# Kernel optimization log

Measured on AMD Instinct MI355X. Metric: run time of the kernel, lower is better.

## Reference

```python
import jax, jax.numpy as jnp
import numpy as np
import math

L = 16
LOGT = 19
T = 2 ** LOGT
F = 2
NMIN = 16
NMAX = 2048
X_MIN = 0.0
X_MAX = 1.0
N_POINTS = 524288
P1 = np.uint32(2654435761)  # spatial hash prime for y
P2 = np.uint32(805459861)   # spatial hash prime for z


def setup_inputs() -> dict:
    key = jax.random.key(0)
    k1, k2 = jax.random.split(key)
    x = jax.random.uniform(k1, (N_POINTS, 3), dtype=jnp.float32)
    hashmap = jax.random.normal(k2, (L, T, F), dtype=jnp.float32) * 1e-2
    b = math.exp((math.log(NMAX) - math.log(NMIN)) / (L - 1))
    resolution = jnp.asarray(np.floor(NMIN * b ** np.arange(L)), dtype=jnp.float32)
    return {"x": x, "hashmap": hashmap, "resolution": resolution}


def reference(x, hashmap, resolution):
    # normalize coords to [0,1] (x_min=0, x_max=1 here)
    xn = (x - X_MIN) / (X_MAX - X_MIN)
    # per-level scaled coords: [L, n, 3]
    xs = xn[None, :, :] * resolution[:, None, None]
    x0f = jnp.floor(xs)
    w = xs - x0f                                 # trilinear weights [L, n, 3]
    c0 = x0f.astype(jnp.uint32)
    c1 = c0 + jnp.uint32(1)
    hx0, hy0, hz0 = c0[..., 0], c0[..., 1] * P1, c0[..., 2] * P2
    hx1, hy1, hz1 = c1[..., 0], c1[..., 1] * P1, c1[..., 2] * P2
    Tm = jnp.uint32(T - 1)
    # 8 corner hash indices, order 000,001,010,011,100,101,110,111: [L, n, 8]
    idx = jnp.stack([
        (hx0 ^ hy0 ^ hz0) & Tm, (hx0 ^ hy0 ^ hz1) & Tm,
        (hx0 ^ hy1 ^ hz0) & Tm, (hx0 ^ hy1 ^ hz1) & Tm,
        (hx1 ^ hy0 ^ hz0) & Tm, (hx1 ^ hy0 ^ hz1) & Tm,
        (hx1 ^ hy1 ^ hz0) & Tm, (hx1 ^ hy1 ^ hz1) & Tm,
    ], axis=-1).astype(jnp.int32)
    wx, wy, wz = w[..., 0], w[..., 1], w[..., 2]
    wxn, wyn, wzn = 1.0 - wx, 1.0 - wy, 1.0 - wz
    # corner weights matching idx order: [L, n, 8]
    cw = jnp.stack([
        wxn * wyn * wzn, wxn * wyn * wz, wxn * wy * wzn, wxn * wy * wz,
        wx * wyn * wzn, wx * wyn * wz, wx * wy * wzn, wx * wy * wz,
    ], axis=-1)
    # gather per-level corner features: [L, n, 8, F]
    feats = jax.vmap(lambda h, i: h[i])(hashmap, idx)
    # interpolate and lay out as [n, L*F] (level-major, matching kernel store)
    out = jnp.einsum('lnc,lncf->nlf', cw, feats)
    return out.reshape(x.shape[0], L * F)
```

## Files before the change

kernel.cpp:

```cpp
#include <hip/hip_runtime.h>
#include <hip/hip_fp16.h>

namespace {
constexpr unsigned kT  = 1u << 19;
constexpr unsigned kTm = kT - 1u;
constexpr unsigned kP1 = 2654435761u;
constexpr unsigned kP2 = 805459861u;
constexpr int      kNPTS = 524288;

constexpr int      kD[5]        = {17, 23, 31, 43, 59};
constexpr unsigned kCellBase[6] = {0u, 4913u, 17080u, 46871u, 126378u, 331757u};
constexpr unsigned kDenseElems4 = 126378u * 8u;
constexpr unsigned kDenseElems5 = 331757u * 8u;
constexpr size_t   kStageBytes  = (size_t)kNPTS * 16u * 8u;
constexpr size_t   kDenseOff    = kStageBytes;
constexpr size_t   kWsNeedB     = kDenseOff + (size_t)kDenseElems4 * 4u;
constexpr size_t   kWsNeedA     = kDenseOff + (size_t)kDenseElems5 * 4u;

constexpr int kDBLK[2]       = {2048, 2560};
constexpr unsigned kMaxBlkV[2] = {3447, 3283};
constexpr int kHSeg[2][8][3][3] = {
 {
  {{ 4,   0,1399},{-1,0,0},{-1,0,0}},
  {{ 4,1399,2048},{ 5,0,2048},{ 6,0, 614}},
  {{ 6, 614,2048},{ 7,0,1877},{-1,0,0}},
  {{ 7,1877,2048},{ 8,0,2048},{ 9,0,1092}},
  {{ 9,1092,2048},{10,0,2048},{11,0, 307}},
  {{11, 307,2048},{12,0,1570},{-1,0,0}},
  {{12,1570,2048},{13,0,2048},{14,0, 785}},
  {{14, 785,2048},{15,0,2048},{-1,0,0}},
 },
 {
  {{ 5,   0, 723},{-1,0,0},{-1,0,0}},
  {{ 5, 723,2048},{ 6,0,1790},{-1,0,0}},
  {{ 6,1790,2048},{ 7,0,2048},{ 8,0, 809}},
  {{ 8, 809,2048},{ 9,0,1876},{-1,0,0}},
  {{ 9,1876,2048},{10,0,2048},{11,0, 895}},
  {{11, 895,2048},{12,0,1962},{-1,0,0}},
  {{12,1962,2048},{13,0,2048},{14,0, 981}},
  {{14, 981,2048},{15,0,2048},{-1,0,0}},
 }};
}

typedef float    f32x2 __attribute__((ext_vector_type(2)));
typedef float    f32x4 __attribute__((ext_vector_type(4)));
typedef unsigned u32x4 __attribute__((ext_vector_type(4)));

__device__ inline f32x2 h2_to_f2(unsigned w) {
    __half2 h = __builtin_bit_cast(__half2, w);
    f32x2 r; r.x = __half2float(h.x); r.y = __half2float(h.y);
    return r;
}

__global__ __launch_bounds__(256) void build_dense16(
    const float* __restrict__ hashmap, unsigned* __restrict__ dense16,
    unsigned elems)
{
    unsigned t = blockIdx.x * 256 + threadIdx.x;
    if (t >= elems) return;
    unsigned cell = t >> 3, corner = t & 7u;
    int l; unsigned rem;
    if      (cell < kCellBase[1]) { l = 0; rem = cell; }
    else if (cell < kCellBase[2]) { l = 1; rem = cell - kCellBase[1]; }
    else if (cell < kCellBase[3]) { l = 2; rem = cell - kCellBase[2]; }
    else if (cell < kCellBase[4]) { l = 3; rem = cell - kCellBase[3]; }
    else                          { l = 4; rem = cell - kCellBase[4]; }
    unsigned D = (unsigned)kD[l];
    unsigned ck = rem % D, tmp = rem / D;
    unsigned cj = tmp % D,  ci = tmp / D;
    unsigned ii = ci + ((corner >> 2) & 1u);
    unsigned jj = cj + ((corner >> 1) & 1u);
    unsigned kk = ck + (corner & 1u);
    unsigned h = (ii ^ (jj * kP1) ^ (kk * kP2)) & kTm;
    f32x2 v = reinterpret_cast<const f32x2*>(hashmap)[(size_t)l * kT + h];
    __half2 p;
    p.x = __float2half_rn(v.x);
    p.y = __float2half_rn(v.y);
    dense16[t] = __builtin_bit_cast(unsigned, p);
}

template <int V>
__global__ __launch_bounds__(256) void hashgrid_gather(
    const float* __restrict__ x,
    const float* __restrict__ hashmap,
    const float* __restrict__ resolution,
    const unsigned* __restrict__ dense16,
    f32x2* __restrict__ stage)
{
    unsigned i = blockIdx.x;
    unsigned g = i & 7u;
    unsigned j = i >> 3;
    unsigned tid = threadIdx.x;

    if (g == 0u && j < (unsigned)kDBLK[V]) {
        unsigned dc0 = j * 4u;
        int l = (int)(dc0 >> 11);
        unsigned c0 = dc0 & 2047u;
        float res = resolution[l];
        unsigned D = (unsigned)kD[l];
        const unsigned* __restrict__ tbl = dense16 + (size_t)kCellBase[l] * 8u;

        #pragma unroll
        for (int p = 0; p < 4; ++p) {
            int n = (int)((c0 + (unsigned)p) * 256u + tid);
            float px = __builtin_nontemporal_load(&x[3*n+0]);
            float py = __builtin_nontemporal_load(&x[3*n+1]);
            float pz = __builtin_nontemporal_load(&x[3*n+2]);
            float xs = px*res, ys = py*res, zs = pz*res;
            float fx = floorf(xs), fy = floorf(ys), fz = floorf(zs);
            float wx = xs-fx, wy = ys-fy, wz = zs-fz;
            unsigned cx0 = (unsigned)fx, cy0 = (unsigned)fy, cz0 = (unsigned)fz;
            unsigned cell = (cx0 * D + cy0) * D + cz0;
            const u32x4* blk = reinterpret_cast<const u32x4*>(tbl + (size_t)cell * 8u);
            u32x4 lo = blk[0], hi = blk[1];
            f32x2 f000 = h2_to_f2(lo.x), f001 = h2_to_f2(lo.y);
            f32x2 f010 = h2_to_f2(lo.z), f011 = h2_to_f2(lo.w);
            f32x2 f100 = h2_to_f2(hi.x), f101 = h2_to_f2(hi.y);
            f32x2 f110 = h2_to_f2(hi.z), f111 = h2_to_f2(hi.w);

            float wxn = 1.f - wx, wyn = 1.f - wy, wzn = 1.f - wz;
            float w000 = wxn*wyn*wzn, w001 = wxn*wyn*wz;
            float w010 = wxn*wy *wzn, w011 = wxn*wy *wz;
            float w100 = wx *wyn*wzn, w101 = wx *wyn*wz;
            float w110 = wx *wy *wzn, w111 = wx *wy *wz;

            f32x2 o;
            o.x = w000*f000.x + w001*f001.x + w010*f010.x + w011*f011.x
                + w100*f100.x + w101*f101.x + w110*f110.x + w111*f111.x;
            o.y = w000*f000.y + w001*f001.y + w010*f010.y + w011*f011.y
                + w100*f100.y + w101*f101.y + w110*f110.y + w111*f111.y;
            __builtin_nontemporal_store(o, &stage[(size_t)l * kNPTS + n]);
        }
        return;
    }

    unsigned jj = (g == 0u) ? j - (unsigned)kDBLK[V] : j;
    int lvl = -1; unsigned chunk = 0, acc = 0;
    #pragma unroll
    for (int s = 0; s < 3; ++s) {
        int l0 = kHSeg[V][g][s][0];
        if (l0 < 0) break;
        unsigned beg = (unsigned)kHSeg[V][g][s][1];
        unsigned len = (unsigned)kHSeg[V][g][s][2] - beg;
        if (jj < acc + len) { lvl = l0; chunk = beg + (jj - acc); break; }
        acc += len;
    }
    if (lvl < 0) return;

    int n = (int)(chunk * 256u + tid);

    float px = __builtin_nontemporal_load(&x[3*n+0]);
    float py = __builtin_nontemporal_load(&x[3*n+1]);
    float pz = __builtin_nontemporal_load(&x[3*n+2]);
    float res = resolution[lvl];

    float xs = px*res, ys = py*res, zs = pz*res;
    float fx = floorf(xs), fy = floorf(ys), fz = floorf(zs);
    float wx = xs-fx, wy = ys-fy, wz = zs-fz;

    unsigned cx0 = (unsigned)fx, cy0 = (unsigned)fy, cz0 = (unsigned)fz;

    f32x2 f000, f001, f010, f011, f100, f101, f110, f111;

    unsigned hy0 = cy0 * kP1, hy1 = (cy0 + 1u) * kP1;
    unsigned hz0 = cz0 * kP2, hz1 = (cz0 + 1u) * kP2;
    unsigned hyz00 = hy0 ^ hz0, hyz01 = hy0 ^ hz1;
    unsigned hyz10 = hy1 ^ hz0, hyz11 = hy1 ^ hz1;
    const f32x2* __restrict__ tb =
        reinterpret_cast<const f32x2*>(hashmap) + (size_t)lvl * kT;

    if ((cx0 & 1u) == 0u) {
        const f32x4* __restrict__ tb4 = reinterpret_cast<const f32x4*>(tb);
        unsigned i00 = (cx0 ^ hyz00) & kTm;
        unsigned i01 = (cx0 ^ hyz01) & kTm;
        unsigned i10 = (cx0 ^ hyz10) & kTm;
        unsigned i11 = (cx0 ^ hyz11) & kTm;
        f32x4 q00 = tb4[i00 >> 1];
        f32x4 q01 = tb4[i01 >> 1];
        f32x4 q10 = tb4[i10 >> 1];
        f32x4 q11 = tb4[i11 >> 1];
        bool o0 = (i00 & 1u), o1 = (i01 & 1u), o2 = (i10 & 1u), o3 = (i11 & 1u);
        f000.x = o0 ? q00.z : q00.x; f000.y = o0 ? q00.w : q00.y;
        f100.x = o0 ? q00.x : q00.z; f100.y = o0 ? q00.y : q00.w;
        f001.x = o1 ? q01.z : q01.x; f001.y = o1 ? q01.w : q01.y;
        f101.x = o1 ? q01.x : q01.z; f101.y = o1 ? q01.y : q01.w;
        f010.x = o2 ? q10.z : q10.x; f010.y = o2 ? q10.w : q10.y;
        f110.x = o2 ? q10.x : q10.z; f110.y = o2 ? q10.y : q10.w;
        f011.x = o3 ? q11.z : q11.x; f011.y = o3 ? q11.w : q11.y;
        f111.x = o3 ? q11.x : q11.z; f111.y = o3 ? q11.y : q11.w;
    } else {
        unsigned hx0 = cx0, hx1 = cx0 + 1u;
        f000 = tb[(hx0 ^ hyz00) & kTm];
        f001 = tb[(hx0 ^ hyz01) & kTm];
        f010 = tb[(hx0 ^ hyz10) & kTm];
        f011 = tb[(hx0 ^ hyz11) & kTm];
        f100 = tb[(hx1 ^ hyz00) & kTm];
        f101 = tb[(hx1 ^ hyz01) & kTm];
        f110 = tb[(hx1 ^ hyz10) & kTm];
        f111 = tb[(hx1 ^ hyz11) & kTm];
    }

    float wxn = 1.f - wx, wyn = 1.f - wy, wzn = 1.f - wz;
    float w000 = wxn*wyn*wzn, w001 = wxn*wyn*wz;
    float w010 = wxn*wy *wzn, w011 = wxn*wy *wz;
    float w100 = wx *wyn*wzn, w101 = wx *wyn*wz;
    float w110 = wx *wy *wzn, w111 = wx *wy *wz;

    f32x2 o;
    o.x = w000*f000.x + w001*f001.x + w010*f010.x + w011*f011.x
        + w100*f100.x + w101*f101.x + w110*f110.x + w111*f111.x;
    o.y = w000*f000.y + w001*f001.y + w010*f010.y + w011*f011.y
        + w100*f100.y + w101*f101.y + w110*f110.y + w111*f111.y;

    __builtin_nontemporal_store(o, &stage[(size_t)lvl * kNPTS + n]);
}

__global__ __launch_bounds__(256) void stage_transpose(
    const f32x2* __restrict__ stage, f32x4* __restrict__ out4)
{
    __shared__ f32x2 tile[128][17];
    unsigned n0 = blockIdx.x * 128u;
    unsigned t = threadIdx.x;

    #pragma unroll
    for (int it = 0; it < 8; ++it) {
        unsigned m = (unsigned)it * 256u + t;
        unsigned l = m >> 7, p = m & 127u;
        tile[p][l] = stage[(size_t)l * kNPTS + n0 + p];
    }
    __syncthreads();

    #pragma unroll
    for (int it = 0; it < 4; ++it) {
        unsigned v = (unsigned)it * 256u + t;
        unsigned p = v >> 3, q = v & 7u;
        f32x2 a = tile[p][2u*q], b = tile[p][2u*q + 1u];
        f32x4 w; w.x = a.x; w.y = a.y; w.z = b.x; w.w = b.y;
        __builtin_nontemporal_store(w, &out4[(size_t)(n0 + p) * 8u + q]);
    }
}

__global__ __launch_bounds__(256) void hashgrid_fwd_lvl(
    const float* __restrict__ x,
    const float* __restrict__ hashmap,
    const float* __restrict__ resolution,
    f32x2* __restrict__ out,
    int npts, unsigned cpl)
{
    unsigned i = blockIdx.x;
    unsigned g = i & 7u;
    unsigned j = i >> 3;
    unsigned phase = j / cpl;
    unsigned chunk = j - phase * cpl;
    unsigned l = g + (phase << 3);

    int n = (int)(chunk * 256u + threadIdx.x);
    if (n >= npts) return;

    float px = x[3*n+0], py = x[3*n+1], pz = x[3*n+2];
    float res = resolution[l];

    float xs = px*res, ys = py*res, zs = pz*res;
    float fx = floorf(xs), fy = floorf(ys), fz = floorf(zs);
    float wx = xs-fx, wy = ys-fy, wz = zs-fz;

    unsigned cx0 = (unsigned)fx, cy0 = (unsigned)fy, cz0 = (unsigned)fz;
    unsigned hx0 = cx0,       hx1 = cx0 + 1u;
    unsigned hy0 = cy0 * kP1, hy1 = (cy0 + 1u) * kP1;
    unsigned hz0 = cz0 * kP2, hz1 = (cz0 + 1u) * kP2;

    const f32x2* __restrict__ tb =
        reinterpret_cast<const f32x2*>(hashmap) + (size_t)l * kT;
    f32x2 f000 = tb[(hx0 ^ hy0 ^ hz0) & kTm];
    f32x2 f001 = tb[(hx0 ^ hy0 ^ hz1) & kTm];
    f32x2 f010 = tb[(hx0 ^ hy1 ^ hz0) & kTm];
    f32x2 f011 = tb[(hx0 ^ hy1 ^ hz1) & kTm];
    f32x2 f100 = tb[(hx1 ^ hy0 ^ hz0) & kTm];
    f32x2 f101 = tb[(hx1 ^ hy0 ^ hz1) & kTm];
    f32x2 f110 = tb[(hx1 ^ hy1 ^ hz0) & kTm];
    f32x2 f111 = tb[(hx1 ^ hy1 ^ hz1) & kTm];

    float wxn = 1.f - wx, wyn = 1.f - wy, wzn = 1.f - wz;
    float w000 = wxn*wyn*wzn, w001 = wxn*wyn*wz;
    float w010 = wxn*wy *wzn, w011 = wxn*wy *wz;
    float w100 = wx *wyn*wzn, w101 = wx *wyn*wz;
    float w110 = wx *wy *wzn, w111 = wx *wy *wz;

    f32x2 o;
    o.x = w000*f000.x + w001*f001.x + w010*f010.x + w011*f011.x
        + w100*f100.x + w101*f101.x + w110*f110.x + w111*f111.x;
    o.y = w000*f000.y + w001*f001.y + w010*f010.y + w011*f011.y
        + w100*f100.y + w101*f101.y + w110*f110.y + w111*f111.y;

    __builtin_nontemporal_store(o, &out[(size_t)n*16 + l]);
}

extern "C" void kernel_launch(void* const* d_in, const int* in_sizes, int n_in,
                              void* d_out, int out_size, void* d_ws, size_t ws_size,
                              hipStream_t stream) {
    const float* x          = (const float*)d_in[0];
    const float* hashmap    = (const float*)d_in[1];
    const float* resolution = (const float*)d_in[2];

    int npts = in_sizes[0] / 3;

    if (npts == kNPTS && d_ws != nullptr && ws_size >= kWsNeedB) {
        bool a = (ws_size >= kWsNeedA);
        f32x2*    stage   = (f32x2*)d_ws;
        unsigned* dense16 = (unsigned*)((char*)d_ws + kDenseOff);
        unsigned elems = a ? kDenseElems5 : kDenseElems4;
        build_dense16<<<(elems + 255u) / 256u, 256, 0, stream>>>(
            hashmap, dense16, elems);
        if (a) {
            hashgrid_gather<1><<<8u * kMaxBlkV[1], 256, 0, stream>>>(
                x, hashmap, resolution, dense16, stage);
        } else {
            hashgrid_gather<0><<<8u * kMaxBlkV[0], 256, 0, stream>>>(
                x, hashmap, resolution, dense16, stage);
        }
        stage_transpose<<<kNPTS / 128, 256, 0, stream>>>(
            stage, (f32x4*)d_out);
    } else {
        unsigned cpl = (unsigned)((npts + 255) / 256);
        unsigned blocks = 16u * cpl;
        hashgrid_fwd_lvl<<<blocks, 256, 0, stream>>>(
            x, hashmap, resolution, (f32x2*)d_out, npts, cpl);
    }
}
```

Baseline: 261.0 us.

## Spread dense-level work evenly across XCDs and drop the fifth dense level

```diff
diff --git a/kernel.cpp b/kernel.cpp
--- a/kernel.cpp
+++ b/kernel.cpp
@@ -8,38 +8,15 @@
 constexpr unsigned kP2 = 805459861u;
 constexpr int      kNPTS = 524288;
 
-constexpr int      kD[5]        = {17, 23, 31, 43, 59};
-constexpr unsigned kCellBase[6] = {0u, 4913u, 17080u, 46871u, 126378u, 331757u};
-constexpr unsigned kDenseElems4 = 126378u * 8u;
-constexpr unsigned kDenseElems5 = 331757u * 8u;
+constexpr int      kD[4]        = {17, 23, 31, 43};
+constexpr unsigned kCellBase[5] = {0u, 4913u, 17080u, 46871u, 126378u};
+constexpr unsigned kDenseElems  = 126378u * 8u;
 constexpr size_t   kStageBytes  = (size_t)kNPTS * 16u * 8u;
 constexpr size_t   kDenseOff    = kStageBytes;
-constexpr size_t   kWsNeedB     = kDenseOff + (size_t)kDenseElems4 * 4u;
-constexpr size_t   kWsNeedA     = kDenseOff + (size_t)kDenseElems5 * 4u;
-
-constexpr int kDBLK[2]       = {2048, 2560};
-constexpr unsigned kMaxBlkV[2] = {3447, 3283};
-constexpr int kHSeg[2][8][3][3] = {
- {
-  {{ 4,   0,1399},{-1,0,0},{-1,0,0}},
-  {{ 4,1399,2048},{ 5,0,2048},{ 6,0, 614}},
-  {{ 6, 614,2048},{ 7,0,1877},{-1,0,0}},
-  {{ 7,1877,2048},{ 8,0,2048},{ 9,0,1092}},
-  {{ 9,1092,2048},{10,0,2048},{11,0, 307}},
-  {{11, 307,2048},{12,0,1570},{-1,0,0}},
-  {{12,1570,2048},{13,0,2048},{14,0, 785}},
-  {{14, 785,2048},{15,0,2048},{-1,0,0}},
- },
- {
-  {{ 5,   0, 723},{-1,0,0},{-1,0,0}},
-  {{ 5, 723,2048},{ 6,0,1790},{-1,0,0}},
-  {{ 6,1790,2048},{ 7,0,2048},{ 8,0, 809}},
-  {{ 8, 809,2048},{ 9,0,1876},{-1,0,0}},
-  {{ 9,1876,2048},{10,0,2048},{11,0, 895}},
-  {{11, 895,2048},{12,0,1962},{-1,0,0}},
-  {{12,1962,2048},{13,0,2048},{14,0, 981}},
-  {{14, 981,2048},{15,0,2048},{-1,0,0}},
- }};
+constexpr size_t   kWsNeed      = kDenseOff + (size_t)kDenseElems * 4u;
+
+constexpr unsigned kDenseBlks    = 256;
+constexpr unsigned kBlocksPerXcd = 3328;
 }
 
 typedef float    f32x2 __attribute__((ext_vector_type(2)));
@@ -53,18 +30,16 @@
 }
 
 __global__ __launch_bounds__(256) void build_dense16(
-    const float* __restrict__ hashmap, unsigned* __restrict__ dense16,
-    unsigned elems)
+    const float* __restrict__ hashmap, unsigned* __restrict__ dense16)
 {
     unsigned t = blockIdx.x * 256 + threadIdx.x;
-    if (t >= elems) return;
+    if (t >= kDenseElems) return;
     unsigned cell = t >> 3, corner = t & 7u;
     int l; unsigned rem;
     if      (cell < kCellBase[1]) { l = 0; rem = cell; }
     else if (cell < kCellBase[2]) { l = 1; rem = cell - kCellBase[1]; }
     else if (cell < kCellBase[3]) { l = 2; rem = cell - kCellBase[2]; }
-    else if (cell < kCellBase[4]) { l = 3; rem = cell - kCellBase[3]; }
-    else                          { l = 4; rem = cell - kCellBase[4]; }
+    else                          { l = 3; rem = cell - kCellBase[3]; }
     unsigned D = (unsigned)kD[l];
     unsigned ck = rem % D, tmp = rem / D;
     unsigned cj = tmp % D,  ci = tmp / D;
@@ -79,7 +54,6 @@
     dense16[t] = __builtin_bit_cast(unsigned, p);
 }
 
-template <int V>
 __global__ __launch_bounds__(256) void hashgrid_gather(
     const float* __restrict__ x,
     const float* __restrict__ hashmap,
@@ -92,10 +66,9 @@
     unsigned j = i >> 3;
     unsigned tid = threadIdx.x;
 
-    if (g == 0u && j < (unsigned)kDBLK[V]) {
-        unsigned dc0 = j * 4u;
-        int l = (int)(dc0 >> 11);
-        unsigned c0 = dc0 & 2047u;
+    if (j < kDenseBlks) {
+        int l = (int)(j >> 6);
+        unsigned c0 = g * 256u + (j & 63u) * 4u;
         float res = resolution[l];
         unsigned D = (unsigned)kD[l];
         const unsigned* __restrict__ tbl = dense16 + (size_t)kCellBase[l] * 8u;
@@ -134,18 +107,9 @@
         return;
     }
 
-    unsigned jj = (g == 0u) ? j - (unsigned)kDBLK[V] : j;
-    int lvl = -1; unsigned chunk = 0, acc = 0;
-    #pragma unroll
-    for (int s = 0; s < 3; ++s) {
-        int l0 = kHSeg[V][g][s][0];
-        if (l0 < 0) break;
-        unsigned beg = (unsigned)kHSeg[V][g][s][1];
-        unsigned len = (unsigned)kHSeg[V][g][s][2] - beg;
-        if (jj < acc + len) { lvl = l0; chunk = beg + (jj - acc); break; }
-        acc += len;
-    }
-    if (lvl < 0) return;
+    unsigned h = g * 3072u + (j - kDenseBlks);
+    int lvl = 4 + (int)(h >> 11);
+    unsigned chunk = h & 2047u;
 
     int n = (int)(chunk * 256u + tid);
 
@@ -304,20 +268,13 @@
 
     int npts = in_sizes[0] / 3;
 
-    if (npts == kNPTS && d_ws != nullptr && ws_size >= kWsNeedB) {
-        bool a = (ws_size >= kWsNeedA);
+    if (npts == kNPTS && d_ws != nullptr && ws_size >= kWsNeed) {
         f32x2*    stage   = (f32x2*)d_ws;
         unsigned* dense16 = (unsigned*)((char*)d_ws + kDenseOff);
-        unsigned elems = a ? kDenseElems5 : kDenseElems4;
-        build_dense16<<<(elems + 255u) / 256u, 256, 0, stream>>>(
-            hashmap, dense16, elems);
-        if (a) {
-            hashgrid_gather<1><<<8u * kMaxBlkV[1], 256, 0, stream>>>(
-                x, hashmap, resolution, dense16, stage);
-        } else {
-            hashgrid_gather<0><<<8u * kMaxBlkV[0], 256, 0, stream>>>(
-                x, hashmap, resolution, dense16, stage);
-        }
+        build_dense16<<<(kDenseElems + 255u) / 256u, 256, 0, stream>>>(
+            hashmap, dense16);
+        hashgrid_gather<<<8u * kBlocksPerXcd, 256, 0, stream>>>(
+            x, hashmap, resolution, dense16, stage);
         stage_transpose<<<kNPTS / 128, 256, 0, stream>>>(
             stage, (f32x4*)d_out);
     } else {
```

Result: faster. 232.2 us (-11.0%).
